# Optimization experiments

Measured on AMD Instinct MI355X. Metric: run time of the kernel, lower is better.

Reference implementation:

```python
import jax, jax.numpy as jnp
import numpy as np

B, S, D, E, F = 2, 2048, 1024, 8, 4096


def setup_inputs() -> dict:
    key = jax.random.key(0)
    k1, k2, k3, k4 = jax.random.split(key, 4)
    x = jax.random.normal(k1, (B, S, D), dtype=jnp.float32)
    gate_w = jax.random.normal(k2, (E, D), dtype=jnp.float32) * 0.02
    w1 = jax.random.normal(k3, (E, D, F), dtype=jnp.float32) * 0.02
    w2 = jax.random.normal(k4, (E, F, D), dtype=jnp.float32) * 0.02
    return {"x": x, "gate_w": gate_w, "w1": w1, "w2": w2}


def reference(x, gate_w, w1, w2):
    b, s, d = x.shape
    n_experts = w1.shape[0]
    tokens = x.reshape(-1, d)                      # (T, D)
    logits = tokens @ gate_w.T                     # (T, E) router (Linear, no bias)
    expert_ids = jnp.argmax(logits, axis=-1)       # top-1 routing (T,)
    dispatch = jax.nn.one_hot(expert_ids, n_experts, dtype=tokens.dtype)  # (T, E)
    # dense all-experts reference of the grouped GEMM: h_e = tokens @ w1[e]
    h = jnp.einsum('td,edf->etf', tokens, w1)      # (E, T, F)
    h = jax.nn.gelu(h, approximate=False)          # torch F.gelu default = exact erf
    out_e = jnp.einsum('etf,efd->etd', h, w2)      # (E, T, D)
    # scatter back: each token takes exactly its assigned expert's output
    out = jnp.einsum('etd,te->td', out_e, dispatch)
    return out.reshape(b, s, d)
```

## Files before the change

### kernel.cpp

```cpp
#include <hip/hip_runtime.h>
#include <math.h>

#define T_TOK 4096
#define D_DIM 1024
#define E_EXP 8
#define F_DIM 4096
#define BM 128
#define BN 128
#define BK 32
#define LDK 40
#define MAX_TILES 40
#define KSPLIT 4

typedef __attribute__((ext_vector_type(8))) short short8;
typedef __attribute__((ext_vector_type(4))) float float4v;

__device__ __forceinline__ short f2b(float f) {
    union { float f; unsigned u; } v; v.f = f;
    unsigned r = v.u + 0x7fffu + ((v.u >> 16) & 1u);
    return (short)(r >> 16);
}

__device__ __forceinline__ void gll16(const short* g, short* l) {
    __builtin_amdgcn_global_load_lds((const __attribute__((address_space(1))) unsigned*)g,
                                     (__attribute__((address_space(3))) unsigned*)l, 16, 0, 0);
}

__global__ void router_kernel(const float* __restrict__ x, const float* __restrict__ gw,
                              short* __restrict__ xb,
                              int* __restrict__ eid, int* __restrict__ rnk,
                              int* __restrict__ counts) {
    int lane = threadIdx.x & 63;
    int wave = threadIdx.x >> 6;
    int t = blockIdx.x * 4 + wave;
    const float* xr = x + (size_t)t * D_DIM;
    float p[E_EXP];
#pragma unroll
    for (int e = 0; e < E_EXP; ++e) p[e] = 0.f;
#pragma unroll
    for (int i = 0; i < D_DIM / 64; ++i) {
        float v = xr[lane + 64 * i];
        if (xb) xb[(size_t)t * D_DIM + lane + 64 * i] = f2b(v);
#pragma unroll
        for (int e = 0; e < E_EXP; ++e)
            p[e] = fmaf(v, gw[e * D_DIM + lane + 64 * i], p[e]);
    }
#pragma unroll
    for (int off = 32; off > 0; off >>= 1) {
#pragma unroll
        for (int e = 0; e < E_EXP; ++e) p[e] += __shfl_down(p[e], off, 64);
    }
    if (lane == 0) {
        int best = 0; float bv = p[0];
#pragma unroll
        for (int e = 1; e < E_EXP; ++e) if (p[e] > bv) { bv = p[e]; best = e; }
        eid[t] = best;
        rnk[t] = atomicAdd(&counts[best], 1);
    }
}

__global__ void prefix_kernel(const int* __restrict__ counts, int* __restrict__ offsets,
                              int* __restrict__ tmap) {
    __shared__ int cnt[E_EXP], off[E_EXP + 1], tp[E_EXP + 1];
    int lane = threadIdx.x;
    if (lane < E_EXP) cnt[lane] = counts[lane];
    __syncthreads();
    if (lane == 0) {
        int o = 0, tv = 0;
        off[0] = 0; tp[0] = 0;
        for (int e = 0; e < E_EXP; ++e) {
            o += cnt[e];
            tv += (cnt[e] + BM - 1) / BM;
            off[e + 1] = o; tp[e + 1] = tv;
        }
    }
    __syncthreads();
    if (lane < E_EXP + 1) offsets[lane] = off[lane];
    if (lane < MAX_TILES) {
        int e = 0;
        while (e < E_EXP && tp[e + 1] <= lane) ++e;
        if (e < E_EXP) {
            int m0 = (lane - tp[e]) * BM;
            int c = cnt[e];
            tmap[lane * 3 + 0] = e;
            tmap[lane * 3 + 1] = off[e] + m0;
            tmap[lane * 3 + 2] = (c - m0 < BM) ? (c - m0) : BM;
        } else {
            tmap[lane * 3 + 2] = 0;
        }
    }
}

__global__ void scatter_kernel(const int* __restrict__ eid, const int* __restrict__ rnk,
                               const int* __restrict__ offsets, int* __restrict__ sorted) {
    int t = blockIdx.x * 256 + threadIdx.x;
    sorted[offsets[eid[t]] + rnk[t]] = t;
}

__global__ __launch_bounds__(256) void tconv_kernel(const float* __restrict__ in,
                                                    short* __restrict__ outp, int R, int C) {
    __shared__ short t[64][72];
    size_t slab = (size_t)R * C;
    const float* ip = in + (size_t)blockIdx.z * slab + (size_t)(blockIdx.y * 64) * C + blockIdx.x * 64;
    short* op = outp + (size_t)blockIdx.z * slab + (size_t)(blockIdx.x * 64) * R + blockIdx.y * 64;
    int tid = threadIdx.x;
    int r = tid >> 2, c4 = (tid & 3) * 16;
    const float* p = ip + (size_t)r * C + c4;
    float4v f0 = *(const float4v*)(p);
    float4v f1 = *(const float4v*)(p + 4);
    float4v f2 = *(const float4v*)(p + 8);
    float4v f3 = *(const float4v*)(p + 12);
#pragma unroll
    for (int j = 0; j < 4; ++j) {
        t[c4 + j][r]      = f2b(f0[j]);
        t[c4 + 4 + j][r]  = f2b(f1[j]);
        t[c4 + 8 + j][r]  = f2b(f2[j]);
        t[c4 + 12 + j][r] = f2b(f3[j]);
    }
    __syncthreads();
    short* q = op + (size_t)r * R + c4;
    *(short8*)q       = *(const short8*)&t[r][c4];
    *(short8*)(q + 8) = *(const short8*)&t[r][c4 + 8];
}

__global__ __launch_bounds__(256) void gemm1_bf16(const short* __restrict__ xb,
                                                  const short* __restrict__ w1b,
                                                  const int* __restrict__ sorted,
                                                  const int* __restrict__ tmap,
                                                  short* __restrict__ hbuf) {
    __shared__ short As[2][BM * BK];
    __shared__ short Bs[2][BN * BK];
    __shared__ int srow[BM];
    int flat = blockIdx.y * 32 + blockIdx.x;
    int swz = (flat & 7) * 160 + (flat >> 3);
    int bx = swz & 31;
    int mt = swz >> 5;
    int m_count = tmap[mt * 3 + 2];
    if (m_count == 0) return;
    int e = tmap[mt * 3 + 0];
    int row0 = tmap[mt * 3 + 1];
    int n0 = bx * BN;
    int tid = threadIdx.x;
    if (tid < BM) srow[tid] = sorted[row0 + (tid < m_count ? tid : m_count - 1)];
    __syncthreads();

    int lane = tid & 63, wave = tid >> 6;
    int wm = (wave & 1) * 64, wn = (wave >> 1) * 64;
    float4v acc[4][4];
#pragma unroll
    for (int i = 0; i < 4; ++i)
#pragma unroll
        for (int j = 0; j < 4; ++j) acc[i][j] = (float4v)(0.f);

    int r0 = wave * 16 + (lane >> 2);
    int r1 = r0 + 64;
    int p0 = ((lane & 3) ^ ((r0 >> 1) & 3)) * 8;
    int p1 = ((lane & 3) ^ ((r1 >> 1) & 3)) * 8;
    const short* ag0 = xb + (size_t)srow[r0] * D_DIM + p0;
    const short* ag1 = xb + (size_t)srow[r1] * D_DIM + p1;
    const short* wb = w1b + (size_t)e * D_DIM * F_DIM;
    const short* bg0 = wb + (size_t)(n0 + r0) * D_DIM + p0;
    const short* bg1 = wb + (size_t)(n0 + r1) * D_DIM + p1;
    int lofs = wave * 512;

    int rfa = lane & 15;
    int clog = lane >> 4;
    int aoff[4], boff[4];
#pragma unroll
    for (int i = 0; i < 4; ++i) {
        int rowa = wm + i * 16 + rfa;
        aoff[i] = rowa * BK + ((clog ^ ((rowa >> 1) & 3)) * 8);
        int rowb = wn + i * 16 + rfa;
        boff[i] = rowb * BK + ((clog ^ ((rowb >> 1) & 3)) * 8);
    }

    gll16(ag0, &As[0][lofs]);
    gll16(ag1, &As[0][lofs + 2048]);
    gll16(bg0, &Bs[0][lofs]);
    gll16(bg1, &Bs[0][lofs + 2048]);
    __syncthreads();

    const int NT = D_DIM / BK;
    int cur = 0;
    for (int t = 0; t < NT; ++t) {
        if (t + 1 < NT) {
            int kn = (t + 1) * BK;
            gll16(ag0 + kn, &As[cur ^ 1][lofs]);
            gll16(ag1 + kn, &As[cur ^ 1][lofs + 2048]);
            gll16(bg0 + kn, &Bs[cur ^ 1][lofs]);
            gll16(bg1 + kn, &Bs[cur ^ 1][lofs + 2048]);
        }
        short8 af[4], bfr[4];
#pragma unroll
        for (int i = 0; i < 4; ++i) af[i] = *(const short8*)(&As[cur][aoff[i]]);
#pragma unroll
        for (int j = 0; j < 4; ++j) bfr[j] = *(const short8*)(&Bs[cur][boff[j]]);
#pragma unroll
        for (int i = 0; i < 4; ++i)
#pragma unroll
            for (int j = 0; j < 4; ++j)
                acc[i][j] = __builtin_amdgcn_mfma_f32_16x16x32_bf16(af[i], bfr[j], acc[i][j], 0, 0, 0);
        __syncthreads();
        cur ^= 1;
    }
    int rbase = (lane >> 4) * 4;
    int cbase = lane & 15;
#pragma unroll
    for (int i = 0; i < 4; ++i) {
#pragma unroll
        for (int r = 0; r < 4; ++r) {
            int row = wm + i * 16 + rbase + r;
            if (row < m_count) {
                short* hp = hbuf + (size_t)(row0 + row) * F_DIM + n0 + wn + cbase;
#pragma unroll
                for (int j = 0; j < 4; ++j) {
                    float s = acc[i][j][r];
                    float g = 0.5f * s * (1.f + erff(s * 0.70710678118f));
                    hp[j * 16] = f2b(g);
                }
            }
        }
    }
}

__global__ __launch_bounds__(256) void gemm2_bf16(const short* __restrict__ hbuf,
                                                  const short* __restrict__ w2b,
                                                  const int* __restrict__ sorted,
                                                  const int* __restrict__ tmap,
                                                  float* __restrict__ out) {
    __shared__ short As[2][BM * BK];
    __shared__ short Bs[2][BN * BK];
    __shared__ int srow[BM];
    int flat = (blockIdx.z * 40 + blockIdx.y) * 8 + blockIdx.x;
    int swz = (flat & 7) * 160 + (flat >> 3);
    int bx = swz & 7;
    int rest = swz >> 3;
    int mt = rest % 40;
    int kz = rest / 40;
    int m_count = tmap[mt * 3 + 2];
    if (m_count == 0) return;
    int e = tmap[mt * 3 + 0];
    int row0 = tmap[mt * 3 + 1];
    int n0 = bx * BN;
    int ks0 = kz * (F_DIM / KSPLIT);
    int tid = threadIdx.x;
    if (tid < BM) srow[tid] = sorted[row0 + (tid < m_count ? tid : m_count - 1)];
    __syncthreads();

    int lane = tid & 63, wave = tid >> 6;
    int wm = (wave & 1) * 64, wn = (wave >> 1) * 64;
    float4v acc[4][4];
#pragma unroll
    for (int i = 0; i < 4; ++i)
#pragma unroll
        for (int j = 0; j < 4; ++j) acc[i][j] = (float4v)(0.f);

    int r0 = wave * 16 + (lane >> 2);
    int r1 = r0 + 64;
    int p0 = ((lane & 3) ^ ((r0 >> 1) & 3)) * 8;
    int p1 = ((lane & 3) ^ ((r1 >> 1) & 3)) * 8;
    int cr0 = r0 < m_count ? r0 : m_count - 1;
    int cr1 = r1 < m_count ? r1 : m_count - 1;
    const short* ag0 = hbuf + (size_t)(row0 + cr0) * F_DIM + ks0 + p0;
    const short* ag1 = hbuf + (size_t)(row0 + cr1) * F_DIM + ks0 + p1;
    const short* wb = w2b + (size_t)e * F_DIM * D_DIM;
    const short* bg0 = wb + (size_t)(n0 + r0) * F_DIM + ks0 + p0;
    const short* bg1 = wb + (size_t)(n0 + r1) * F_DIM + ks0 + p1;
    int lofs = wave * 512;

    int rfa = lane & 15;
    int clog = lane >> 4;
    int aoff[4], boff[4];
#pragma unroll
    for (int i = 0; i < 4; ++i) {
        int rowa = wm + i * 16 + rfa;
        aoff[i] = rowa * BK + ((clog ^ ((rowa >> 1) & 3)) * 8);
        int rowb = wn + i * 16 + rfa;
        boff[i] = rowb * BK + ((clog ^ ((rowb >> 1) & 3)) * 8);
    }

    gll16(ag0, &As[0][lofs]);
    gll16(ag1, &As[0][lofs + 2048]);
    gll16(bg0, &Bs[0][lofs]);
    gll16(bg1, &Bs[0][lofs + 2048]);
    __syncthreads();

    const int NT = (F_DIM / KSPLIT) / BK;
    int cur = 0;
    for (int t = 0; t < NT; ++t) {
        if (t + 1 < NT) {
            int kn = (t + 1) * BK;
            gll16(ag0 + kn, &As[cur ^ 1][lofs]);
            gll16(ag1 + kn, &As[cur ^ 1][lofs + 2048]);
            gll16(bg0 + kn, &Bs[cur ^ 1][lofs]);
            gll16(bg1 + kn, &Bs[cur ^ 1][lofs + 2048]);
        }
        short8 af[4], bfr[4];
#pragma unroll
        for (int i = 0; i < 4; ++i) af[i] = *(const short8*)(&As[cur][aoff[i]]);
#pragma unroll
        for (int j = 0; j < 4; ++j) bfr[j] = *(const short8*)(&Bs[cur][boff[j]]);
#pragma unroll
        for (int i = 0; i < 4; ++i)
#pragma unroll
            for (int j = 0; j < 4; ++j)
                acc[i][j] = __builtin_amdgcn_mfma_f32_16x16x32_bf16(af[i], bfr[j], acc[i][j], 0, 0, 0);
        __syncthreads();
        cur ^= 1;
    }
    int rbase = (lane >> 4) * 4;
    int cbase = lane & 15;
#pragma unroll
    for (int i = 0; i < 4; ++i) {
#pragma unroll
        for (int r = 0; r < 4; ++r) {
            int row = wm + i * 16 + rbase + r;
            if (row < m_count) {
                float* op = out + (size_t)srow[row] * D_DIM + n0 + wn + cbase;
#pragma unroll
                for (int j = 0; j < 4; ++j) atomicAdd(op + j * 16, acc[i][j][r]);
            }
        }
    }
}

__global__ __launch_bounds__(256) void gemm1_kernel(const float* __restrict__ x,
                                                    const float* __restrict__ w1,
                                                    const int* __restrict__ sorted,
                                                    const int* __restrict__ tmap,
                                                    short* __restrict__ hbuf) {
    __shared__ short As[BM * LDK];
    __shared__ short Bs[BN * LDK];
    __shared__ int srow[BM];
    int mt = blockIdx.y;
    int m_count = tmap[mt * 3 + 2];
    if (m_count == 0) return;
    int e = tmap[mt * 3 + 0];
    int row0 = tmap[mt * 3 + 1];
    int n0 = blockIdx.x * BN;
    int tid = threadIdx.x;
    if (tid < BM) srow[tid] = sorted[row0 + (tid < m_count ? tid : m_count - 1)];
    __syncthreads();

    int lane = tid & 63, wave = tid >> 6;
    int wm = (wave & 1) * 64, wn = (wave >> 1) * 64;
    float4v acc[4][4];
#pragma unroll
    for (int i = 0; i < 4; ++i)
#pragma unroll
        for (int j = 0; j < 4; ++j) acc[i][j] = (float4v)(0.f);

    int ar = tid >> 1;
    int ac = (tid & 1) * 16;
    int bn = tid & 127;
    int bq = (tid >> 7) * 16;
    const float* abase = x + (size_t)srow[ar] * D_DIM + ac;
    const float* bbase = w1 + (size_t)e * D_DIM * F_DIM + (size_t)bq * F_DIM + (n0 + bn);

    for (int k0 = 0; k0 < D_DIM; k0 += BK) {
        {
            const float* ap = abase + k0;
            float4v f0 = *(const float4v*)(ap);
            float4v f1 = *(const float4v*)(ap + 4);
            float4v f2 = *(const float4v*)(ap + 8);
            float4v f3 = *(const float4v*)(ap + 12);
            short8 s0, s1;
#pragma unroll
            for (int c = 0; c < 4; ++c) {
                s0[c] = f2b(f0[c]); s0[4 + c] = f2b(f1[c]);
                s1[c] = f2b(f2[c]); s1[4 + c] = f2b(f3[c]);
            }
            *(short8*)(&As[ar * LDK + ac]) = s0;
            *(short8*)(&As[ar * LDK + ac + 8]) = s1;
        }
        {
            const float* bp = bbase + (size_t)k0 * F_DIM;
            float v[16];
#pragma unroll
            for (int j = 0; j < 16; ++j) v[j] = bp[(size_t)j * F_DIM];
            short8 s0, s1;
#pragma unroll
            for (int j = 0; j < 8; ++j) { s0[j] = f2b(v[j]); s1[j] = f2b(v[8 + j]); }
            *(short8*)(&Bs[bn * LDK + bq]) = s0;
            *(short8*)(&Bs[bn * LDK + bq + 8]) = s1;
        }
        __syncthreads();
        short8 af[4], bfr[4];
#pragma unroll
        for (int i = 0; i < 4; ++i)
            af[i] = *(const short8*)(&As[(wm + i * 16 + (lane & 15)) * LDK + (lane >> 4) * 8]);
#pragma unroll
        for (int j = 0; j < 4; ++j)
            bfr[j] = *(const short8*)(&Bs[(wn + j * 16 + (lane & 15)) * LDK + (lane >> 4) * 8]);
#pragma unroll
        for (int i = 0; i < 4; ++i)
#pragma unroll
            for (int j = 0; j < 4; ++j)
                acc[i][j] = __builtin_amdgcn_mfma_f32_16x16x32_bf16(af[i], bfr[j], acc[i][j], 0, 0, 0);
        __syncthreads();
    }
    int rbase = (lane >> 4) * 4;
    int cbase = lane & 15;
#pragma unroll
    for (int i = 0; i < 4; ++i) {
#pragma unroll
        for (int r = 0; r < 4; ++r) {
            int row = wm + i * 16 + rbase + r;
            if (row < m_count) {
                short* hp = hbuf + (size_t)(row0 + row) * F_DIM + n0 + wn + cbase;
#pragma unroll
                for (int j = 0; j < 4; ++j) {
                    float s = acc[i][j][r];
                    float g = 0.5f * s * (1.f + erff(s * 0.70710678118f));
                    hp[j * 16] = f2b(g);
                }
            }
        }
    }
}

__global__ __launch_bounds__(256) void gemm2_kernel(const short* __restrict__ hbuf,
                                                    const float* __restrict__ w2,
                                                    const int* __restrict__ sorted,
                                                    const int* __restrict__ tmap,
                                                    float* __restrict__ out) {
    __shared__ short As[BM * LDK];
    __shared__ short Bs[BN * LDK];
    __shared__ int srow[BM];
    int mt = blockIdx.y;
    int m_count = tmap[mt * 3 + 2];
    if (m_count == 0) return;
    int e = tmap[mt * 3 + 0];
    int row0 = tmap[mt * 3 + 1];
    int n0 = blockIdx.x * BN;
    int tid = threadIdx.x;
    if (tid < BM) srow[tid] = sorted[row0 + (tid < m_count ? tid : m_count - 1)];
    __syncthreads();

    int lane = tid & 63, wave = tid >> 6;
    int wm = (wave & 1) * 64, wn = (wave >> 1) * 64;
    float4v acc[4][4];
#pragma unroll
    for (int i = 0; i < 4; ++i)
#pragma unroll
        for (int j = 0; j < 4; ++j) acc[i][j] = (float4v)(0.f);

    int ar = tid >> 1;
    int ac = (tid & 1) * 16;
    int bn = tid & 127;
    int bq = (tid >> 7) * 16;
    int arc = ar < m_count ? ar : m_count - 1;
    const short* abase = hbuf + (size_t)(row0 + arc) * F_DIM + ac;
    const float* bbase = w2 + (size_t)e * F_DIM * D_DIM + (size_t)bq * D_DIM + (n0 + bn);

    for (int k0 = 0; k0 < F_DIM; k0 += BK) {
        {
            const short* ap = abase + k0;
            *(short8*)(&As[ar * LDK + ac]) = *(const short8*)(ap);
            *(short8*)(&As[ar * LDK + ac + 8]) = *(const short8*)(ap + 8);
        }
        {
            const float* bp = bbase + (size_t)k0 * D_DIM;
            float v[16];
#pragma unroll
            for (int j = 0; j < 16; ++j) v[j] = bp[(size_t)j * D_DIM];
            short8 s0, s1;
#pragma unroll
            for (int j = 0; j < 8; ++j) { s0[j] = f2b(v[j]); s1[j] = f2b(v[8 + j]); }
            *(short8*)(&Bs[bn * LDK + bq]) = s0;
            *(short8*)(&Bs[bn * LDK + bq + 8]) = s1;
        }
        __syncthreads();
        short8 af[4], bfr[4];
#pragma unroll
        for (int i = 0; i < 4; ++i)
            af[i] = *(const short8*)(&As[(wm + i * 16 + (lane & 15)) * LDK + (lane >> 4) * 8]);
#pragma unroll
        for (int j = 0; j < 4; ++j)
            bfr[j] = *(const short8*)(&Bs[(wn + j * 16 + (lane & 15)) * LDK + (lane >> 4) * 8]);
#pragma unroll
        for (int i = 0; i < 4; ++i)
#pragma unroll
            for (int j = 0; j < 4; ++j)
                acc[i][j] = __builtin_amdgcn_mfma_f32_16x16x32_bf16(af[i], bfr[j], acc[i][j], 0, 0, 0);
        __syncthreads();
    }
    int rbase = (lane >> 4) * 4;
    int cbase = lane & 15;
#pragma unroll
    for (int i = 0; i < 4; ++i) {
#pragma unroll
        for (int r = 0; r < 4; ++r) {
            int row = wm + i * 16 + rbase + r;
            if (row < m_count) {
                float* op = out + (size_t)srow[row] * D_DIM + n0 + wn + cbase;
#pragma unroll
                for (int j = 0; j < 4; ++j) op[j * 16] = acc[i][j][r];
            }
        }
    }
}

extern "C" void kernel_launch(void* const* d_in, const int* in_sizes, int n_in,
                              void* d_out, int out_size, void* d_ws, size_t ws_size,
                              hipStream_t stream) {
    const float* x  = (const float*)d_in[0];
    const float* gw = (const float*)d_in[1];
    const float* w1 = (const float*)d_in[2];
    const float* w2 = (const float*)d_in[3];
    float* out = (float*)d_out;
    char* ws = (char*)d_ws;

    int* counts  = (int*)(ws);
    int* offsets = (int*)(ws + 64);
    int* tmap    = (int*)(ws + 128);
    int* eid     = (int*)(ws + 1024);
    int* rnk     = (int*)(ws + 17408);
    int* sorted  = (int*)(ws + 33792);
    short* hbuf  = (short*)(ws + 51200);

    const size_t HB  = 33554432ull;
    const size_t XB  = 8388608ull;
    const size_t WB  = 67108864ull;
    short* xb  = (short*)(ws + 51200 + HB);
    short* w1b = (short*)(ws + 51200 + HB + XB);
    short* w2b = (short*)(ws + 51200 + HB + XB + WB);
    const size_t need = 51200ull + HB + XB + 2ull * WB;
    bool fast = ws_size >= need;

    hipMemsetAsync(counts, 0, 32, stream);
    router_kernel<<<T_TOK / 4, 256, 0, stream>>>(x, gw, fast ? xb : (short*)0, eid, rnk, counts);

    if (fast) {
        hipMemsetAsync(out, 0, (size_t)T_TOK * D_DIM * 4, stream);
        tconv_kernel<<<dim3(F_DIM / 64, D_DIM / 64, E_EXP), 256, 0, stream>>>(w1, w1b, D_DIM, F_DIM);
        tconv_kernel<<<dim3(D_DIM / 64, F_DIM / 64, E_EXP), 256, 0, stream>>>(w2, w2b, F_DIM, D_DIM);
    }

    prefix_kernel<<<1, 64, 0, stream>>>(counts, offsets, tmap);
    scatter_kernel<<<T_TOK / 256, 256, 0, stream>>>(eid, rnk, offsets, sorted);

    if (fast) {
        gemm1_bf16<<<dim3(F_DIM / BN, MAX_TILES), 256, 0, stream>>>(xb, w1b, sorted, tmap, hbuf);
        gemm2_bf16<<<dim3(D_DIM / BN, MAX_TILES, KSPLIT), 256, 0, stream>>>(hbuf, w2b, sorted, tmap, out);
    } else {
        gemm1_kernel<<<dim3(F_DIM / BN, MAX_TILES), 256, 0, stream>>>(x, w1, sorted, tmap, hbuf);
        gemm2_kernel<<<dim3(D_DIM / BN, MAX_TILES), 256, 0, stream>>>(hbuf, w2, sorted, tmap, out);
    }
}
```

Measured before the change: 574.2 us.

## Triple-buffer LDS tiles with explicit vmcnt waits in both expert GEMMs

Both grouped GEMM kernels switch from double to triple buffered LDS, keeping two K-tiles of global-to-LDS loads in flight. The full __syncthreads drain is replaced by partial s_waitcnt vmcnt counts plus raw s_barrier and sched_barrier fences. The aim is to hide global memory latency behind the MFMA work. In exchange, LDS use per block grows by half, which may reduce occupancy, and correctness now depends on the hand-written vmcnt counts matching the number of outstanding loads.

```diff
diff --git a/kernel.cpp b/kernel.cpp
--- a/kernel.cpp
+++ b/kernel.cpp
@@ -8,6 +8,7 @@
 #define BM 128
 #define BN 128
 #define BK 32
+#define BUFE (BM * BK)
 #define LDK 40
 #define MAX_TILES 40
 #define KSPLIT 4
@@ -128,8 +129,8 @@
                                                   const int* __restrict__ sorted,
                                                   const int* __restrict__ tmap,
                                                   short* __restrict__ hbuf) {
-    __shared__ short As[2][BM * BK];
-    __shared__ short Bs[2][BN * BK];
+    __shared__ short As[3 * BUFE];
+    __shared__ short Bs[3 * BUFE];
     __shared__ int srow[BM];
     int flat = blockIdx.y * 32 + blockIdx.x;
     int swz = (flat & 7) * 160 + (flat >> 3);
@@ -174,34 +175,48 @@
         boff[i] = rowb * BK + ((clog ^ ((rowb >> 1) & 3)) * 8);
     }
 
-    gll16(ag0, &As[0][lofs]);
-    gll16(ag1, &As[0][lofs + 2048]);
-    gll16(bg0, &Bs[0][lofs]);
-    gll16(bg1, &Bs[0][lofs + 2048]);
-    __syncthreads();
+    gll16(ag0,      As + lofs);
+    gll16(ag1,      As + lofs + 2048);
+    gll16(bg0,      Bs + lofs);
+    gll16(bg1,      Bs + lofs + 2048);
+    gll16(ag0 + BK, As + BUFE + lofs);
+    gll16(ag1 + BK, As + BUFE + lofs + 2048);
+    gll16(bg0 + BK, Bs + BUFE + lofs);
+    gll16(bg1 + BK, Bs + BUFE + lofs + 2048);
 
     const int NT = D_DIM / BK;
-    int cur = 0;
+    int cur = 0, nxt = 2;
     for (int t = 0; t < NT; ++t) {
-        if (t + 1 < NT) {
-            int kn = (t + 1) * BK;
-            gll16(ag0 + kn, &As[cur ^ 1][lofs]);
-            gll16(ag1 + kn, &As[cur ^ 1][lofs + 2048]);
-            gll16(bg0 + kn, &Bs[cur ^ 1][lofs]);
-            gll16(bg1 + kn, &Bs[cur ^ 1][lofs + 2048]);
-        }
+        if (t + 2 < NT) {
+            int kn = (t + 2) * BK;
+            int no = nxt * BUFE + lofs;
+            gll16(ag0 + kn, As + no);
+            gll16(ag1 + kn, As + no + 2048);
+            gll16(bg0 + kn, Bs + no);
+            gll16(bg1 + kn, Bs + no + 2048);
+        }
+        __builtin_amdgcn_sched_barrier(0);
+        if (t + 2 < NT)      asm volatile("s_waitcnt vmcnt(8)" ::: "memory");
+        else if (t + 1 < NT) asm volatile("s_waitcnt vmcnt(4)" ::: "memory");
+        else                 asm volatile("s_waitcnt vmcnt(0)" ::: "memory");
+        __builtin_amdgcn_sched_barrier(0);
+        __builtin_amdgcn_s_barrier();
+        __builtin_amdgcn_sched_barrier(0);
+        int co = cur * BUFE;
         short8 af[4], bfr[4];
 #pragma unroll
-        for (int i = 0; i < 4; ++i) af[i] = *(const short8*)(&As[cur][aoff[i]]);
-#pragma unroll
-        for (int j = 0; j < 4; ++j) bfr[j] = *(const short8*)(&Bs[cur][boff[j]]);
+        for (int i = 0; i < 4; ++i) af[i] = *(const short8*)(&As[co + aoff[i]]);
+#pragma unroll
+        for (int j = 0; j < 4; ++j) bfr[j] = *(const short8*)(&Bs[co + boff[j]]);
 #pragma unroll
         for (int i = 0; i < 4; ++i)
 #pragma unroll
             for (int j = 0; j < 4; ++j)
                 acc[i][j] = __builtin_amdgcn_mfma_f32_16x16x32_bf16(af[i], bfr[j], acc[i][j], 0, 0, 0);
-        __syncthreads();
-        cur ^= 1;
+        __builtin_amdgcn_s_barrier();
+        __builtin_amdgcn_sched_barrier(0);
+        cur = (cur == 2) ? 0 : cur + 1;
+        nxt = (nxt == 2) ? 0 : nxt + 1;
     }
     int rbase = (lane >> 4) * 4;
     int cbase = lane & 15;
@@ -228,8 +243,8 @@
                                                   const int* __restrict__ sorted,
                                                   const int* __restrict__ tmap,
                                                   float* __restrict__ out) {
-    __shared__ short As[2][BM * BK];
-    __shared__ short Bs[2][BN * BK];
+    __shared__ short As[3 * BUFE];
+    __shared__ short Bs[3 * BUFE];
     __shared__ int srow[BM];
     int flat = (blockIdx.z * 40 + blockIdx.y) * 8 + blockIdx.x;
     int swz = (flat & 7) * 160 + (flat >> 3);
@@ -279,34 +294,48 @@
         boff[i] = rowb * BK + ((clog ^ ((rowb >> 1) & 3)) * 8);
     }
 
-    gll16(ag0, &As[0][lofs]);
-    gll16(ag1, &As[0][lofs + 2048]);
-    gll16(bg0, &Bs[0][lofs]);
-    gll16(bg1, &Bs[0][lofs + 2048]);
-    __syncthreads();
+    gll16(ag0,      As + lofs);
+    gll16(ag1,      As + lofs + 2048);
+    gll16(bg0,      Bs + lofs);
+    gll16(bg1,      Bs + lofs + 2048);
+    gll16(ag0 + BK, As + BUFE + lofs);
+    gll16(ag1 + BK, As + BUFE + lofs + 2048);
+    gll16(bg0 + BK, Bs + BUFE + lofs);
+    gll16(bg1 + BK, Bs + BUFE + lofs + 2048);
 
     const int NT = (F_DIM / KSPLIT) / BK;
-    int cur = 0;
+    int cur = 0, nxt = 2;
     for (int t = 0; t < NT; ++t) {
-        if (t + 1 < NT) {
-            int kn = (t + 1) * BK;
-            gll16(ag0 + kn, &As[cur ^ 1][lofs]);
-            gll16(ag1 + kn, &As[cur ^ 1][lofs + 2048]);
-            gll16(bg0 + kn, &Bs[cur ^ 1][lofs]);
-            gll16(bg1 + kn, &Bs[cur ^ 1][lofs + 2048]);
-        }
+        if (t + 2 < NT) {
+            int kn = (t + 2) * BK;
+            int no = nxt * BUFE + lofs;
+            gll16(ag0 + kn, As + no);
+            gll16(ag1 + kn, As + no + 2048);
+            gll16(bg0 + kn, Bs + no);
+            gll16(bg1 + kn, Bs + no + 2048);
+        }
+        __builtin_amdgcn_sched_barrier(0);
+        if (t + 2 < NT)      asm volatile("s_waitcnt vmcnt(8)" ::: "memory");
+        else if (t + 1 < NT) asm volatile("s_waitcnt vmcnt(4)" ::: "memory");
+        else                 asm volatile("s_waitcnt vmcnt(0)" ::: "memory");
+        __builtin_amdgcn_sched_barrier(0);
+        __builtin_amdgcn_s_barrier();
+        __builtin_amdgcn_sched_barrier(0);
+        int co = cur * BUFE;
         short8 af[4], bfr[4];
 #pragma unroll
-        for (int i = 0; i < 4; ++i) af[i] = *(const short8*)(&As[cur][aoff[i]]);
-#pragma unroll
-        for (int j = 0; j < 4; ++j) bfr[j] = *(const short8*)(&Bs[cur][boff[j]]);
+        for (int i = 0; i < 4; ++i) af[i] = *(const short8*)(&As[co + aoff[i]]);
+#pragma unroll
+        for (int j = 0; j < 4; ++j) bfr[j] = *(const short8*)(&Bs[co + boff[j]]);
 #pragma unroll
         for (int i = 0; i < 4; ++i)
 #pragma unroll
             for (int j = 0; j < 4; ++j)
                 acc[i][j] = __builtin_amdgcn_mfma_f32_16x16x32_bf16(af[i], bfr[j], acc[i][j], 0, 0, 0);
-        __syncthreads();
-        cur ^= 1;
+        __builtin_amdgcn_s_barrier();
+        __builtin_amdgcn_sched_barrier(0);
+        cur = (cur == 2) ? 0 : cur + 1;
+        nxt = (nxt == 2) ? 0 : nxt + 1;
     }
     int rbase = (lane >> 4) * 4;
     int cbase = lane & 15;
```

Result: faster. 560.2 us (-2.4%).
